# Kernel tuning notes

Hardware: AMD Instinct MI355X
Metric: run time of the kernel (lower is better)

Reference implementation:

```python
import jax, jax.numpy as jnp
import numpy as np

DIM = 384
DIM_HEAD = 384
HEADS = 4
SCALE = (DIM_HEAD / HEADS) ** -0.5  # per-head dim 96


def _chan_layernorm(x, g, eps=1e-5):
    # LayerNorm over channel dim (axis=1), biased variance, scale only
    mean = jnp.mean(x, axis=1, keepdims=True)
    var = jnp.var(x, axis=1, keepdims=True)
    return (x - mean) * jax.lax.rsqrt(var + eps) * g


def setup_inputs() -> dict:
    key = jax.random.key(0)
    k0, k1, k2 = jax.random.split(key, 3)
    x = jax.random.normal(k0, (16, DIM, 64, 64), dtype=jnp.float32)
    prenorm_g = jnp.ones((1, DIM, 1, 1), dtype=jnp.float32)
    Wqkv = jax.random.normal(k1, (3 * DIM_HEAD, DIM), dtype=jnp.float32) * 0.02
    Wout = jax.random.normal(k2, (DIM, DIM_HEAD), dtype=jnp.float32) * 0.02
    bout = jnp.zeros((DIM,), dtype=jnp.float32)
    outnorm_g = jnp.ones((1, DIM, 1, 1), dtype=jnp.float32)
    return {"x": x, "prenorm_g": prenorm_g, "Wqkv": Wqkv,
            "Wout": Wout, "bout": bout, "outnorm_g": outnorm_g}


def reference(x, prenorm_g, Wqkv, Wout, bout, outnorm_g):
    b, c, h, w = x.shape
    n = h * w
    ch = DIM_HEAD // HEADS  # per-head channels

    xn = _chan_layernorm(x, prenorm_g)              # prenorm; residual uses this
    qkv = jnp.einsum('oc,bchw->bohw', Wqkv, xn)     # 1x1 conv, no bias
    q, k, v = jnp.split(qkv, 3, axis=1)             # each [b, dim_head, h, w]

    def to_heads(t):
        return t.reshape(b, HEADS, ch, n)           # b h c (x y)
    q, k, v = to_heads(q), to_heads(k), to_heads(v)

    q = jax.nn.softmax(q, axis=2) * SCALE           # softmax over channel dim
    k = jax.nn.softmax(k, axis=3)                   # softmax over spatial dim

    context = jnp.einsum('bhdn,bhen->bhde', k, v)   # [b,h,ch,ch]
    out = jnp.einsum('bhde,bhdn->bhen', context, q) # [b,h,ch,n]
    out = out.reshape(b, DIM_HEAD, h, w)

    out = jnp.einsum('oc,bchw->bohw', Wout, out) + bout[None, :, None, None]
    out = _chan_layernorm(out, outnorm_g)
    return out + xn
```

## Files before the change

kernel.cpp:

```cpp
#include <hip/hip_runtime.h>
#include <cstdint>
#include <cstddef>


#define P_     65536
#define P96_   6291456
#define ROW_   384
#define NS_    8
#define CHK_   512
#define SCALE_ 0.10206207261596577f
#define EPS_   1e-5f

typedef unsigned short us16;
typedef __attribute__((ext_vector_type(8))) unsigned short ushort8;
typedef __attribute__((ext_vector_type(8))) short short8;
typedef __attribute__((ext_vector_type(4))) float f32x4;
typedef __attribute__((ext_vector_type(2))) unsigned int uint2v;

static __device__ __forceinline__ float bfu2f(us16 u) {
  union { float f; unsigned int i; } x; x.i = ((unsigned int)u) << 16; return x.f;
}
static __device__ __forceinline__ us16 f2bfu(float f) {
  union { float f; unsigned int u; } x; x.f = f;
  unsigned int r = x.u + 0x7fffu + ((x.u >> 16) & 1u);
  return (us16)(r >> 16);
}

#define GLDS16(gp, lp) \
  __builtin_amdgcn_global_load_lds((const __attribute__((address_space(1))) void*)(gp), \
                                   (__attribute__((address_space(3))) void*)(lp), 16, 0, 0)

__global__ __launch_bounds__(256) void k_wcvt(const float* __restrict__ wqkv,
                                              const float* __restrict__ wout,
                                              us16* __restrict__ wbf) {
  int i = (blockIdx.x * 256 + threadIdx.x) * 4;
  const float* s = (i < 442368) ? (wqkv + i) : (wout + (i - 442368));
  wbf[i + 0] = f2bfu(s[0]); wbf[i + 1] = f2bfu(s[1]);
  wbf[i + 2] = f2bfu(s[2]); wbf[i + 3] = f2bfu(s[3]);
}

__global__ __launch_bounds__(256) void k_prenorm(const float* __restrict__ x,
                                                 const float* __restrict__ g,
                                                 us16* __restrict__ xn) {
  __shared__ float gs[384];
  __shared__ float sm[4][64], sq[4][64];
  int t = threadIdx.x;
  for (int c = t; c < 384; c += 256) gs[c] = g[c];
  int qd = t >> 6, pb = t & 63;
  int p = blockIdx.x * 64 + pb;
  int b = p >> 12, pix = p & 4095;
  const float* xb = x + (size_t)b * 1572864 + pix;
  float xv[96];
  float s1 = 0.f, s2 = 0.f;
  #pragma unroll
  for (int i = 0; i < 96; ++i) {
    float v = xb[(size_t)(qd * 96 + i) * 4096];
    xv[i] = v; s1 += v; s2 += v * v;
  }
  sm[qd][pb] = s1; sq[qd][pb] = s2;
  __syncthreads();
  float su = sm[0][pb] + sm[1][pb] + sm[2][pb] + sm[3][pb];
  float ss = sq[0][pb] + sq[1][pb] + sq[2][pb] + sq[3][pb];
  float mean = su * (1.f / 384);
  float var = ss * (1.f / 384) - mean * mean;
  float rs = rsqrtf(var + EPS_);
  us16* ob = xn + (size_t)p * ROW_ + qd * 96;
  #pragma unroll
  for (int c8 = 0; c8 < 12; ++c8) {
    ushort8 u;
    #pragma unroll
    for (int j = 0; j < 8; ++j)
      u[j] = f2bfu((xv[c8 * 8 + j] - mean) * rs * gs[qd * 96 + c8 * 8 + j]);
    *(ushort8*)(ob + c8 * 8) = u;
  }
}

__global__ __launch_bounds__(512, 2) void k_gemm(const us16* __restrict__ src,
                                                 const us16* __restrict__ W,
                                                 us16* __restrict__ dst,
                                                 int MT, int mode) {
  __shared__ __align__(16) us16 As[3 * 16384];
  __shared__ __align__(16) us16 Bs[3 * 8192];
  int i = blockIdx.x;
  int xcd = i & 7, idx = i >> 3;
  int ot = idx % MT;
  int pt = (idx / MT) * 8 + xcd;
  int p0 = pt * 256, o0 = ot * 128;
  int tid = threadIdx.x;
  int wv = tid >> 6, l = tid & 63;
  int wr = wv >> 1, wc = wv & 1;
  int lm = l & 15, kq = l >> 4;
  int lr = l >> 3, lg = l & 7;

  bool rm = (mode != 0) || (ot < 3);
  bool isk = (mode == 0) && (ot >= 3) && (ot < 6);
  const us16* Wb = (mode != 0) ? (W + (size_t)(p0 >> 12) * 147456) : W;

  const us16* aB[4]; const us16* bB[2];
  int swz = (lg ^ lr) * 8;
  #pragma unroll
  for (int r = 0; r < 4; ++r)
    aB[r] = src + (size_t)(p0 + 64 * r + 8 * wv + lr) * ROW_ + swz;
  #pragma unroll
  for (int r = 0; r < 2; ++r)
    bB[r] = Wb + (size_t)(o0 + 64 * r + 8 * wv + lr) * ROW_ + swz;

  int aidx[4][2], bidx[4][2];
  #pragma unroll
  for (int ii = 0; ii < 4; ++ii) {
    int row = wr * 64 + ii * 16 + lm;
    #pragma unroll
    for (int ks = 0; ks < 2; ++ks)
      aidx[ii][ks] = row * 8 + ((ks * 4 + kq) ^ (row & 7));
  }
  #pragma unroll
  for (int jj = 0; jj < 4; ++jj) {
    int row = wc * 64 + jj * 16 + lm;
    #pragma unroll
    for (int ks = 0; ks < 2; ++ks)
      bidx[jj][ks] = row * 8 + ((ks * 4 + kq) ^ (row & 7));
  }

  f32x4 acc[4][4];
  #pragma unroll
  for (int a = 0; a < 4; ++a)
    #pragma unroll
    for (int q = 0; q < 4; ++q) acc[a][q] = (f32x4)0.f;

#define STG(t_, b_) do { \
    _Pragma("unroll") \
    for (int r_ = 0; r_ < 4; ++r_) \
      GLDS16(aB[r_] + (t_) * 64, &As[(b_) * 16384 + (64 * r_ + 8 * wv) * 64]); \
    _Pragma("unroll") \
    for (int r_ = 0; r_ < 2; ++r_) \
      GLDS16(bB[r_] + (t_) * 64, &Bs[(b_) * 8192 + (64 * r_ + 8 * wv) * 64]); \
  } while (0)

  STG(0, 0);
  STG(1, 1);
  asm volatile("s_waitcnt vmcnt(6)\n\ts_barrier" ::: "memory");

  #pragma unroll
  for (int t = 0; t < 6; ++t) {
    if (t + 2 < 6) STG(t + 2, (t + 2) % 3);
    const short8* A8 = (const short8*)As + (t % 3) * 2048;
    const short8* B8 = (const short8*)Bs + (t % 3) * 1024;
    __builtin_amdgcn_s_setprio(1);
    #pragma unroll
    for (int ks = 0; ks < 2; ++ks) {
      short8 af[4], bf[4];
      #pragma unroll
      for (int ii = 0; ii < 4; ++ii) af[ii] = A8[aidx[ii][ks]];
      #pragma unroll
      for (int jj = 0; jj < 4; ++jj) bf[jj] = B8[bidx[jj][ks]];
      if (rm) {
        #pragma unroll
        for (int ii = 0; ii < 4; ++ii)
          #pragma unroll
          for (int jj = 0; jj < 4; ++jj)
            acc[ii][jj] = __builtin_amdgcn_mfma_f32_16x16x32_bf16(bf[jj], af[ii], acc[ii][jj], 0, 0, 0);
      } else {
        #pragma unroll
        for (int ii = 0; ii < 4; ++ii)
          #pragma unroll
          for (int jj = 0; jj < 4; ++jj)
            acc[ii][jj] = __builtin_amdgcn_mfma_f32_16x16x32_bf16(af[ii], bf[jj], acc[ii][jj], 0, 0, 0);
      }
    }
    __builtin_amdgcn_s_setprio(0);
    if (t < 5) {
      if (t + 2 < 6)
        asm volatile("s_waitcnt vmcnt(6) lgkmcnt(0)\n\ts_barrier" ::: "memory");
      else
        asm volatile("s_waitcnt vmcnt(0) lgkmcnt(0)\n\ts_barrier" ::: "memory");
    }
  }
#undef STG

  __syncthreads();
  us16* Cs = As;
  const int MS = rm ? 136 : 264;
  #pragma unroll
  for (int ii = 0; ii < 4; ++ii) {
    #pragma unroll
    for (int jj = 0; jj < 4; ++jj) {
      f32x4 v = acc[ii][jj];
      if (isk) {
        #pragma unroll
        for (int r = 0; r < 4; ++r) v[r] = __expf(v[r]);
      }
      alignas(8) us16 b4[4];
      #pragma unroll
      for (int r = 0; r < 4; ++r) b4[r] = f2bfu(v[r]);
      int maj = rm ? (wr * 64 + ii * 16 + lm) : (wc * 64 + jj * 16 + lm);
      int mnr = rm ? (wc * 64 + jj * 16 + kq * 4) : (wr * 64 + ii * 16 + kq * 4);
      *(uint2v*)&Cs[maj * MS + mnr] = *(const uint2v*)b4;
    }
  }
  __syncthreads();

  if (!rm) {
    #pragma unroll
    for (int it = 0; it < 8; ++it) {
      int c = it * 512 + tid;
      int o_l = c >> 5, p8 = c & 31;
      int o = o0 + o_l, sec = o / 96, d = o - sec * 96;
      ushort8 u = *(const ushort8*)&Cs[o_l * 264 + p8 * 8];
      *(ushort8*)(dst + (size_t)sec * P96_ + (size_t)d * P_ + p0 + p8 * 8) = u;
    }
  } else if (mode) {
    #pragma unroll
    for (int it = 0; it < 8; ++it) {
      int c = it * 512 + tid;
      int p_l = c >> 4, ch = c & 15;
      ushort8 u = *(const ushort8*)&Cs[p_l * 136 + ch * 8];
      *(ushort8*)(dst + (size_t)(p0 + p_l) * ROW_ + o0 + ch * 8) = u;
    }
  } else {
    #pragma unroll
    for (int it = 0; it < 8; ++it) {
      int c = it * 512 + tid;
      int p_l = c >> 4, ch = c & 15;
      int o = o0 + ch * 8, sec = o / 96, d = o - sec * 96;
      ushort8 u = *(const ushort8*)&Cs[p_l * 136 + ch * 8];
      *(ushort8*)(dst + (size_t)sec * P96_ + (size_t)(p0 + p_l) * 96 + d) = u;
    }
  }
}

__global__ __launch_bounds__(256) void k_ctx(const us16* __restrict__ qkv,
                                             float* __restrict__ ctxs,
                                             float* __restrict__ zs) {
  __shared__ __align__(16) us16 Ek[96 * 64];
  __shared__ __align__(16) us16 Vv[96 * 64];
  int bh = blockIdx.x, s = blockIdx.y;
  int b = bh >> 2, h = bh & 3;
  const us16* kb = qkv + (size_t)(4 + h) * P96_;
  const us16* vb = qkv + (size_t)(8 + h) * P96_;
  int pbase = b * 4096 + s * CHK_;
  int t = threadIdx.x;
  int wv = t >> 6, l = t & 63;
  int wr = wv >> 1, wc = wv & 1;
  int lm = l & 15, kq = l >> 4;

  f32x4 acc[3][3];
  f32x4 accz[3];
  #pragma unroll
  for (int a = 0; a < 3; ++a) {
    accz[a] = (f32x4)0.f;
    #pragma unroll
    for (int q = 0; q < 3; ++q) acc[a][q] = (f32x4)0.f;
  }
  short8 vone;
  #pragma unroll
  for (int j = 0; j < 8; ++j) vone[j] = (short)0x3F80;

  int srow = wv * 24 + (l >> 3);
  int sgrp = l & 7;

  for (int tile = 0; tile < CHK_ / 64; ++tile) {
    int p0 = pbase + tile * 64;
    #pragma unroll
    for (int c = 0; c < 3; ++c) {
      int r = srow + c * 8;
      int g = sgrp ^ (r & 7);
      GLDS16(kb + (size_t)r * P_ + p0 + g * 8, &Ek[(wv * 24 + c * 8) * 64]);
      GLDS16(vb + (size_t)r * P_ + p0 + g * 8, &Vv[(wv * 24 + c * 8) * 64]);
    }
    __syncthreads();
    const short8* A8 = (const short8*)Ek;
    const short8* B8 = (const short8*)Vv;
    #pragma unroll
    for (int ks = 0; ks < 2; ++ks) {
      short8 af[3], bf[3];
      #pragma unroll
      for (int ii = 0; ii < 3; ++ii) {
        int m = wr * 48 + ii * 16 + lm;
        af[ii] = A8[m * 8 + (((ks * 4 + kq) ^ m) & 7) + ((ks * 4 + kq) & 8)];
        int e = wc * 48 + ii * 16 + lm;
        bf[ii] = B8[e * 8 + (((ks * 4 + kq) ^ e) & 7) + ((ks * 4 + kq) & 8)];
      }
      #pragma unroll
      for (int ii = 0; ii < 3; ++ii)
        #pragma unroll
        for (int jj = 0; jj < 3; ++jj)
          acc[ii][jj] = __builtin_amdgcn_mfma_f32_16x16x32_bf16(af[ii], bf[jj], acc[ii][jj], 0, 0, 0);
      if (wc == 0) {
        #pragma unroll
        for (int ii = 0; ii < 3; ++ii)
          accz[ii] = __builtin_amdgcn_mfma_f32_16x16x32_bf16(af[ii], vone, accz[ii], 0, 0, 0);
      }
    }
    __syncthreads();
  }

  float* cb = ctxs + (size_t)(s * 64 + bh) * 9216;
  #pragma unroll
  for (int ii = 0; ii < 3; ++ii) {
    int m0 = wr * 48 + ii * 16 + kq * 4;
    #pragma unroll
    for (int jj = 0; jj < 3; ++jj) {
      int e = wc * 48 + jj * 16 + lm;
      #pragma unroll
      for (int r = 0; r < 4; ++r)
        cb[(size_t)(m0 + r) * 96 + e] = acc[ii][jj][r];
    }
  }
  if (wc == 0 && lm == 0) {
    #pragma unroll
    for (int ii = 0; ii < 3; ++ii) {
      int m0 = wr * 48 + ii * 16 + kq * 4;
      #pragma unroll
      for (int r = 0; r < 4; ++r)
        zs[(size_t)(s * 64 + bh) * 96 + m0 + r] = accz[ii][r];
    }
  }
}

__global__ __launch_bounds__(256) void k_ctxred(const float* __restrict__ ctxs,
                                                const float* __restrict__ zs,
                                                float* __restrict__ ctx,
                                                float* __restrict__ zr) {
  int bh = blockIdx.x / 9, part = blockIdx.x % 9;
  int t = threadIdx.x;
  int idx = part * 1024 + t * 4;
  f32x4 sum = (f32x4)0.f;
  #pragma unroll
  for (int s = 0; s < NS_; ++s)
    sum += *(const f32x4*)&ctxs[(size_t)(s * 64 + bh) * 9216 + idx];
  *(f32x4*)&ctx[(size_t)bh * 9216 + idx] = sum;
  if (part == 0 && t < 96) {
    float z = 0.f;
    #pragma unroll
    for (int s = 0; s < NS_; ++s) z += zs[(size_t)(s * 64 + bh) * 96 + t];
    zr[bh * 96 + t] = z;
  }
}

__global__ __launch_bounds__(256) void k_ctxw(const float* __restrict__ ctx,
                                              const float* __restrict__ zr,
                                              const us16* __restrict__ wout,
                                              us16* __restrict__ Mt) {
  __shared__ __align__(16) us16 Aw[192 * 104];
  __shared__ __align__(16) us16 Bh[96 * 104];
  __shared__ __align__(16) us16 Bl[96 * 104];
  int bh = blockIdx.x >> 1, half = blockIdx.x & 1;
  int b = bh >> 2, h = bh & 3;
  int o0 = half * 192;
  int t = threadIdx.x;

  #pragma unroll
  for (int it = 0; it < 9; ++it) {
    int c = it * 256 + t;
    int row = c / 12, e8 = c % 12;
    ushort8 u = *(const ushort8*)(wout + (size_t)(o0 + row) * 384 + h * 96 + e8 * 8);
    *(ushort8*)&Aw[row * 104 + e8 * 8] = u;
  }
  const float* cb = ctx + (size_t)bh * 9216;
  #pragma unroll
  for (int it = 0; it < 9; ++it) {
    int c = it * 256 + t;
    int fi = c * 4;
    int row = fi / 96, e = fi % 96;
    f32x4 v = *(const f32x4*)&cb[fi];
    alignas(8) us16 hi[4], lo[4];
    #pragma unroll
    for (int r = 0; r < 4; ++r) {
      hi[r] = f2bfu(v[r]);
      lo[r] = f2bfu(v[r] - bfu2f(hi[r]));
    }
    *(uint2v*)&Bh[row * 104 + e] = *(const uint2v*)hi;
    *(uint2v*)&Bl[row * 104 + e] = *(const uint2v*)lo;
  }
  __syncthreads();

  int wv = t >> 6, l = t & 63;
  int lm = l & 15, kq = l >> 4;
  f32x4 acc[3][6];
  #pragma unroll
  for (int a = 0; a < 3; ++a)
    #pragma unroll
    for (int q = 0; q < 6; ++q) acc[a][q] = (f32x4)0.f;

  const short8* A8 = (const short8*)Aw;
  const short8* B8h = (const short8*)Bh;
  const short8* B8l = (const short8*)Bl;
  #pragma unroll
  for (int ks = 0; ks < 3; ++ks) {
    short8 af[3];
    #pragma unroll
    for (int ii = 0; ii < 3; ++ii)
      af[ii] = A8[(wv * 48 + ii * 16 + lm) * 13 + ks * 4 + kq];
    #pragma unroll
    for (int jj = 0; jj < 6; ++jj) {
      short8 bh8 = B8h[(jj * 16 + lm) * 13 + ks * 4 + kq];
      short8 bl8 = B8l[(jj * 16 + lm) * 13 + ks * 4 + kq];
      #pragma unroll
      for (int ii = 0; ii < 3; ++ii) {
        acc[ii][jj] = __builtin_amdgcn_mfma_f32_16x16x32_bf16(af[ii], bh8, acc[ii][jj], 0, 0, 0);
        acc[ii][jj] = __builtin_amdgcn_mfma_f32_16x16x32_bf16(af[ii], bl8, acc[ii][jj], 0, 0, 0);
      }
    }
  }

  us16* mb = Mt + (size_t)b * 147456;
  #pragma unroll
  for (int jj = 0; jj < 6; ++jj) {
    int d = jj * 16 + lm;
    float zinv = 1.0f / zr[bh * 96 + d];
    #pragma unroll
    for (int ii = 0; ii < 3; ++ii) {
      int orow = o0 + wv * 48 + ii * 16 + kq * 4;
      #pragma unroll
      for (int r = 0; r < 4; ++r)
        mb[(size_t)(orow + r) * 384 + h * 96 + d] = f2bfu(acc[ii][jj][r] * zinv);
    }
  }
}

__global__ __launch_bounds__(256) void k_qsm(const us16* __restrict__ qkv,
                                             us16* __restrict__ Qp) {
  int p = blockIdx.x * 256 + threadIdx.x;
  #pragma unroll 1
  for (int h = 0; h < 4; ++h) {
    const us16* qrow = qkv + (size_t)h * P96_ + (size_t)p * 96;
    float qv[96];
    #pragma unroll
    for (int c8 = 0; c8 < 12; ++c8) {
      ushort8 u = *(const ushort8*)(qrow + c8 * 8);
      #pragma unroll
      for (int j = 0; j < 8; ++j) qv[c8 * 8 + j] = bfu2f(u[j]);
    }
    float m = -1e30f;
    #pragma unroll
    for (int d = 0; d < 96; ++d) m = fmaxf(m, qv[d]);
    float s = 0.f;
    #pragma unroll
    for (int d = 0; d < 96; ++d) { qv[d] = __expf(qv[d] - m); s += qv[d]; }
    float sc = SCALE_ / s;
    us16* ob = Qp + (size_t)p * ROW_ + h * 96;
    #pragma unroll
    for (int c8 = 0; c8 < 12; ++c8) {
      ushort8 u;
      #pragma unroll
      for (int j = 0; j < 8; ++j) u[j] = f2bfu(qv[c8 * 8 + j] * sc);
      *(ushort8*)(ob + c8 * 8) = u;
    }
  }
}

__global__ __launch_bounds__(256) void k_outnorm(const us16* __restrict__ y,
                                                 const us16* __restrict__ xn,
                                                 const float* __restrict__ bout,
                                                 const float* __restrict__ g,
                                                 float* __restrict__ out) {
  __shared__ float bs[384], gs[384];
  int t = threadIdx.x;
  for (int c = t; c < 384; c += 256) { bs[c] = bout[c]; gs[c] = g[c]; }
  __syncthreads();
  int p = blockIdx.x * 256 + t;
  int b = p >> 12, pix = p & 4095;
  const us16* yb = y + (size_t)p * ROW_;
  const us16* xb = xn + (size_t)p * ROW_;
  float sum = 0.f, sq = 0.f;
  #pragma unroll 4
  for (int c8 = 0; c8 < 48; ++c8) {
    ushort8 u = *(const ushort8*)(yb + c8 * 8);
    #pragma unroll
    for (int j = 0; j < 8; ++j) {
      float v = bfu2f(u[j]) + bs[c8 * 8 + j];
      sum += v; sq += v * v;
    }
  }
  float mean = sum * (1.f / 384);
  float var = sq * (1.f / 384) - mean * mean;
  float rs = rsqrtf(var + EPS_);
  float* oB = out + (size_t)b * 1572864 + pix;
  #pragma unroll 2
  for (int c8 = 0; c8 < 48; ++c8) {
    ushort8 u = *(const ushort8*)(yb + c8 * 8);
    ushort8 ux = *(const ushort8*)(xb + c8 * 8);
    #pragma unroll
    for (int j = 0; j < 8; ++j) {
      int c = c8 * 8 + j;
      float v = bfu2f(u[j]) + bs[c];
      oB[(size_t)c * 4096] = (v - mean) * rs * gs[c] + bfu2f(ux[j]);
    }
  }
}

extern "C" void kernel_launch(void* const* d_in, const int* in_sizes, int n_in,
                              void* d_out, int out_size, void* d_ws, size_t ws_size,
                              hipStream_t stream) {
  const float* x    = (const float*)d_in[0];
  const float* pg   = (const float*)d_in[1];
  const float* wqkv = (const float*)d_in[2];
  const float* wout = (const float*)d_in[3];
  const float* bout = (const float*)d_in[4];
  const float* og   = (const float*)d_in[5];

  char* ws = (char*)d_ws;
  us16*  xn     = (us16*)(ws);
  us16*  qkv    = (us16*)(ws + 50331648);
  us16*  Qp     = (us16*)(ws + 201326592);
  float* ctxred = (float*)(ws + 251658240);
  float* zred   = (float*)(ws + 254017536);
  us16*  wbf    = (us16*)(ws + 254042112);
  us16*  y      = qkv;
  float* out    = (float*)d_out;
  float* ctxs = (float*)d_out;
  float* zs   = (float*)((char*)d_out + 18874368);
  us16*  Mt   = (us16*)((char*)d_out + 19070976);

  k_wcvt<<<576, 256, 0, stream>>>(wqkv, wout, wbf);
  k_prenorm<<<1024, 256, 0, stream>>>(x, pg, xn);
  k_gemm<<<2304, 512, 0, stream>>>(xn, wbf, qkv, 9, 0);
  k_ctx<<<dim3(64, NS_), 256, 0, stream>>>(qkv, ctxs, zs);
  k_ctxred<<<576, 256, 0, stream>>>(ctxs, zs, ctxred, zred);
  k_ctxw<<<128, 256, 0, stream>>>(ctxred, zred, wbf + 442368, Mt);
  k_qsm<<<256, 256, 0, stream>>>(qkv, Qp);
  k_gemm<<<768, 512, 0, stream>>>(Qp, Mt, y, 3, 1);
  k_outnorm<<<256, 256, 0, stream>>>(y, xn, bout, og, out);
}
```

Before: 434.7 us.

## Halve GEMM K-tile to 32 to shrink LDS and raise occupancy

The GEMM kernel's K-step is cut from 64 to 32 elements, so the triple-buffered LDS drops from about 144KB to 72KB. Launch bounds move from 2 to 4 blocks per CU, with a new swizzle and index scheme fitted to 32-wide rows. The intent is more resident waves to hide memory latency. In exchange the loop runs 12 iterations instead of 6, which doubles the barriers per tile, and register pressure under the 4-block bound may cause spills.

Result: slower. 901.8 us (+107.5%).

```diff
diff --git a/kernel.cpp b/kernel.cpp
--- a/kernel.cpp
+++ b/kernel.cpp
@@ -75,12 +75,11 @@
   }
 }
 
-__global__ __launch_bounds__(512, 2) void k_gemm(const us16* __restrict__ src,
+__global__ __launch_bounds__(512, 4) void k_gemm(const us16* __restrict__ src,
                                                  const us16* __restrict__ W,
                                                  us16* __restrict__ dst,
                                                  int MT, int mode) {
-  __shared__ __align__(16) us16 As[3 * 16384];
-  __shared__ __align__(16) us16 Bs[3 * 8192];
+  __shared__ __align__(16) us16 LDS[36864];
   int i = blockIdx.x;
   int xcd = i & 7, idx = i >> 3;
   int ot = idx % MT;
@@ -90,36 +89,25 @@
   int wv = tid >> 6, l = tid & 63;
   int wr = wv >> 1, wc = wv & 1;
   int lm = l & 15, kq = l >> 4;
-  int lr = l >> 3, lg = l & 7;
 
   bool rm = (mode != 0) || (ot < 3);
   bool isk = (mode == 0) && (ot >= 3) && (ot < 6);
   const us16* Wb = (mode != 0) ? (W + (size_t)(p0 >> 12) * 147456) : W;
 
-  const us16* aB[4]; const us16* bB[2];
-  int swz = (lg ^ lr) * 8;
-  #pragma unroll
-  for (int r = 0; r < 4; ++r)
-    aB[r] = src + (size_t)(p0 + 64 * r + 8 * wv + lr) * ROW_ + swz;
-  #pragma unroll
-  for (int r = 0; r < 2; ++r)
-    bB[r] = Wb + (size_t)(o0 + 64 * r + 8 * wv + lr) * ROW_ + swz;
-
-  int aidx[4][2], bidx[4][2];
-  #pragma unroll
-  for (int ii = 0; ii < 4; ++ii) {
-    int row = wr * 64 + ii * 16 + lm;
-    #pragma unroll
-    for (int ks = 0; ks < 2; ++ks)
-      aidx[ii][ks] = row * 8 + ((ks * 4 + kq) ^ (row & 7));
-  }
-  #pragma unroll
-  for (int jj = 0; jj < 4; ++jj) {
-    int row = wc * 64 + jj * 16 + lm;
-    #pragma unroll
-    for (int ks = 0; ks < 2; ++ks)
-      bidx[jj][ks] = row * 8 + ((ks * 4 + kq) ^ (row & 7));
-  }
+  int srow = l >> 2;
+  int swz = ((l & 3) ^ ((l >> 3) & 3)) * 8;
+  const us16* aB0 = src + (size_t)(p0 + wv * 32 + srow) * ROW_ + swz;
+  const us16* aB1 = src + (size_t)(p0 + wv * 32 + 16 + srow) * ROW_ + swz;
+  const us16* bB  = Wb  + (size_t)(o0 + wv * 16 + srow) * ROW_ + swz;
+
+  int fswz = (lm >> 1) & 3;
+  int aidx[4], bidx[4];
+  #pragma unroll
+  for (int ii = 0; ii < 4; ++ii)
+    aidx[ii] = (wr * 64 + ii * 16 + lm) * 4 + (kq ^ fswz);
+  #pragma unroll
+  for (int jj = 0; jj < 4; ++jj)
+    bidx[jj] = (wc * 64 + jj * 16 + lm) * 4 + (kq ^ fswz);
 
   f32x4 acc[4][4];
   #pragma unroll
@@ -127,32 +115,28 @@
     #pragma unroll
     for (int q = 0; q < 4; ++q) acc[a][q] = (f32x4)0.f;
 
-#define STG(t_, b_) do { \
-    _Pragma("unroll") \
-    for (int r_ = 0; r_ < 4; ++r_) \
-      GLDS16(aB[r_] + (t_) * 64, &As[(b_) * 16384 + (64 * r_ + 8 * wv) * 64]); \
-    _Pragma("unroll") \
-    for (int r_ = 0; r_ < 2; ++r_) \
-      GLDS16(bB[r_] + (t_) * 64, &Bs[(b_) * 8192 + (64 * r_ + 8 * wv) * 64]); \
+#define STG(t_, s_) do { \
+    GLDS16(aB0 + (t_) * 32, &LDS[(s_) * 12288 + (wv * 32) * 32]); \
+    GLDS16(aB1 + (t_) * 32, &LDS[(s_) * 12288 + (wv * 32 + 16) * 32]); \
+    GLDS16(bB  + (t_) * 32, &LDS[(s_) * 12288 + 8192 + (wv * 16) * 32]); \
   } while (0)
 
   STG(0, 0);
   STG(1, 1);
-  asm volatile("s_waitcnt vmcnt(6)\n\ts_barrier" ::: "memory");
-
-  #pragma unroll
-  for (int t = 0; t < 6; ++t) {
-    if (t + 2 < 6) STG(t + 2, (t + 2) % 3);
-    const short8* A8 = (const short8*)As + (t % 3) * 2048;
-    const short8* B8 = (const short8*)Bs + (t % 3) * 1024;
+  asm volatile("s_waitcnt vmcnt(3)\n\ts_barrier" ::: "memory");
+
+  #pragma unroll
+  for (int t = 0; t < 12; ++t) {
+    if (t + 2 < 12) STG(t + 2, (t + 2) % 3);
+    const short8* A8 = (const short8*)(LDS + (t % 3) * 12288);
+    const short8* B8 = (const short8*)(LDS + (t % 3) * 12288 + 8192);
     __builtin_amdgcn_s_setprio(1);
-    #pragma unroll
-    for (int ks = 0; ks < 2; ++ks) {
+    {
       short8 af[4], bf[4];
       #pragma unroll
-      for (int ii = 0; ii < 4; ++ii) af[ii] = A8[aidx[ii][ks]];
-      #pragma unroll
-      for (int jj = 0; jj < 4; ++jj) bf[jj] = B8[bidx[jj][ks]];
+      for (int ii = 0; ii < 4; ++ii) af[ii] = A8[aidx[ii]];
+      #pragma unroll
+      for (int jj = 0; jj < 4; ++jj) bf[jj] = B8[bidx[jj]];
       if (rm) {
         #pragma unroll
         for (int ii = 0; ii < 4; ++ii)
@@ -168,9 +152,9 @@
       }
     }
     __builtin_amdgcn_s_setprio(0);
-    if (t < 5) {
-      if (t + 2 < 6)
-        asm volatile("s_waitcnt vmcnt(6) lgkmcnt(0)\n\ts_barrier" ::: "memory");
+    if (t < 11) {
+      if (t + 2 < 12)
+        asm volatile("s_waitcnt vmcnt(3) lgkmcnt(0)\n\ts_barrier" ::: "memory");
       else
         asm volatile("s_waitcnt vmcnt(0) lgkmcnt(0)\n\ts_barrier" ::: "memory");
     }
@@ -178,7 +162,7 @@
 #undef STG
 
   __syncthreads();
-  us16* Cs = As;
+  us16* Cs = LDS;
   const int MS = rm ? 136 : 264;
   #pragma unroll
   for (int ii = 0; ii < 4; ++ii) {
```
